# Optimization experiments

Hardware: AMD Instinct MI355X
Metric: run time of the kernel (lower is better)

Reference implementation:

```python
import jax, jax.numpy as jnp
import numpy as np


def setup_inputs() -> dict:
    key = jax.random.key(0)
    k1, k2 = jax.random.split(key)
    flow = jax.random.normal(k1, (4, 2, 256, 256), dtype=jnp.float32)   # [B,2,H,W] per-pixel flow over dt
    spike = jax.random.uniform(k2, (4, 64, 256, 256), dtype=jnp.float32)  # [B,C,H,W] spike voxel grid
    return {"flow": flow, "spike": spike}


def _splat(vals, xn, yn, H, W):
    """Forward bilinear splat of vals [H,W] to continuous coords (xn,yn) [H,W]."""
    x0 = jnp.floor(xn)
    y0 = jnp.floor(yn)
    wx = xn - x0  # fractional weights (differentiable w.r.t. flow)
    wy = yn - y0
    x0i = x0.astype(jnp.int32)
    y0i = y0.astype(jnp.int32)
    out = jnp.zeros(H * W, dtype=vals.dtype)
    corners = (
        (0, 0, (1.0 - wx) * (1.0 - wy)),
        (1, 0, wx * (1.0 - wy)),
        (0, 1, (1.0 - wx) * wy),
        (1, 1, wx * wy),
    )
    for dx, dy, w in corners:
        xi = x0i + dx
        yi = y0i + dy
        valid = (xi >= 0) & (xi < W) & (yi >= 0) & (yi < H)
        idx = jnp.clip(yi, 0, H - 1) * W + jnp.clip(xi, 0, W - 1)
        out = out.at[idx.ravel()].add(jnp.where(valid, w * vals, 0.0).ravel())
    return out.reshape(H, W)


def spike_warp_mid(spike, flow, dt):
    """Warp each time bin c by flow * (c - mid)/dt toward the middle timestamp (bilinear splat)."""
    B, C, H, W = spike.shape
    mid = (C - 1) / 2.0
    yy, xx = jnp.meshgrid(jnp.arange(H, dtype=spike.dtype),
                          jnp.arange(W, dtype=spike.dtype), indexing='ij')
    s = (jnp.arange(C, dtype=spike.dtype) - mid) / jnp.asarray(dt, spike.dtype)  # [C]
    u = flow[:, 0][:, None]  # [B,1,H,W]
    v = flow[:, 1][:, None]
    xn = xx + u * s[None, :, None, None]  # [B,C,H,W]
    yn = yy + v * s[None, :, None, None]
    splat_bc = jax.vmap(jax.vmap(lambda va, xa, ya: _splat(va, xa, ya, H, W)))
    return splat_bc(spike, xn, yn)  # [B,C,H,W]


def reference(flow, spike):
    B, C, H, W = spike.shape
    spike_warped = spike_warp_mid(spike, flow, dt=64)
    # Faithful to original: sum over BATCH dim inside per-batch loop (same each iter),
    # so loss = (B * -var) / B = -var(spike_image) with unbiased variance.
    spike_image = jnp.sum(spike_warped, axis=0)  # [C,H,W]
    loss = -jnp.var(spike_image - jnp.mean(spike_image), ddof=1)
    return loss
```

## Files before the change

kernel.cpp:

```cpp
#include <hip/hip_runtime.h>

typedef float f2 __attribute__((ext_vector_type(2)));
typedef float f4v __attribute__((ext_vector_type(4)));

constexpr int B = 4, C = 64, H = 256, W = 256;
constexpr int HW = H * W;
constexpr long long N_TOT = (long long)C * HW;

constexpr int TS = 16;
constexpr int PPS = 19;
constexpr int PPA = PPS * 18;
constexpr int OVW = 17;
constexpr int OVA = OVW * OVW;
constexpr int NBLK = 2048;

__global__ __launch_bounds__(256) void fused_kernel(
    const float* __restrict__ flow,
    const float* __restrict__ spike,
    double* __restrict__ partials) {
  __shared__ __align__(16) f4v pl01[PPA];
  __shared__ __align__(16) f4v pl23[PPA];
  __shared__ f2 uvp[PPA];
  __shared__ __align__(16) float ovf[8 * OVA];
  __shared__ double red[8];

  const int bid = blockIdx.x;
  const int part = bid >> 3;
  const int j = 7 - ((bid ^ (bid >> 3)) & 7);
  const int tx0 = (part & 15) * TS;
  const int ty0 = (part >> 4) * TS;
  const int tid = threadIdx.x;
  const int qx = tid & 15, qy = tid >> 4;
  const int wave = tid >> 6;

  {
    f4v z = {0.f, 0.f, 0.f, 0.f};
    f4v* ov4 = (f4v*)ovf;
    for (int i = tid; i < (8 * OVA) / 4; i += 256) ov4[i] = z;
  }

  f2 smv[4];
#pragma unroll
  for (int t = 0; t < 4; ++t) {
    float s = ((float)(4 * j + t) + 0.5f) * (1.0f / 64.0f);
    smv[t] = f2{-s, s};
  }
  const int cn0 = 31 - 4 * j;
  const int cp0 = 32 + 4 * j;
  const int Rj = (j >> 1) + 1;
  const int SWj = TS + 2 * Rj;
  const int SAj = SWj * SWj;
  const int sbg = (ty0 - Rj) * W + (tx0 - Rj);

  int c_rc[3];
  int c_meta[3];
#pragma unroll
  for (int k = 0; k < 3; ++k) {
    int pos = tid + 256 * k;
    bool act = pos < SAj;
    int row = act ? pos / SWj : 0;
    int col = pos - row * SWj;
    int relx = col - Rj, rely = row - Rj;
    int gy = ty0 + rely, gx = tx0 + relx;
    bool val = act & ((unsigned)gy < (unsigned)H) & ((unsigned)gx < (unsigned)W);
    bool inn = act & (relx >= -1) & (relx <= 16) & (rely >= -1) & (rely <= 16);
    c_rc[k] = (row << 8) | col;
    c_meta[k] = (int)act | ((int)val << 1) | ((int)inn << 2);
  }

  __syncthreads();

  const int qb = (qy + 1) * PPS + (qx + 1);
  f2 acc2[4];
#pragma unroll
  for (int t = 0; t < 4; ++t) acc2[t] = f2{0.f, 0.f};

  for (int bb = 0; bb < B; ++bb) {
    const float* fu = flow + (size_t)bb * 2 * HW;
    const float* fv = fu + HW;
    const float* spb = spike + (size_t)bb * C * HW;

#pragma unroll
    for (int k = 0; k < 3; ++k) {
      const int meta = c_meta[k];
      if (!(meta & 1)) continue;
      const int row = c_rc[k] >> 8, col = c_rc[k] & 255;
      const int gp = sbg + c_rc[k];
      const bool valb = (meta & 2) != 0;
      const bool innb = (meta & 4) != 0;
      float u = 0.f, v = 0.f;
      if (valb) { u = fu[gp]; v = fv[gp]; }
      const float es = fmaxf(fabsf(u), fabsf(v));
      const bool ev0 = es * smv[0].y >= 1.0f;
      const bool ev1 = es * smv[1].y >= 1.0f;
      const bool ev2 = es * smv[2].y >= 1.0f;
      const bool ev3 = es * smv[3].y >= 1.0f;
      float n0 = 0.f, n1 = 0.f, n2 = 0.f, n3 = 0.f;
      float p0 = 0.f, p1 = 0.f, p2 = 0.f, p3 = 0.f;
      if (valb && (innb || ev3)) {
        n0 = spb[(size_t)cn0 * HW + gp];
        n1 = spb[(size_t)(cn0 - 1) * HW + gp];
        n2 = spb[(size_t)(cn0 - 2) * HW + gp];
        n3 = spb[(size_t)(cn0 - 3) * HW + gp];
        p0 = spb[(size_t)cp0 * HW + gp];
        p1 = spb[(size_t)(cp0 + 1) * HW + gp];
        p2 = spb[(size_t)(cp0 + 2) * HW + gp];
        p3 = spb[(size_t)(cp0 + 3) * HW + gp];
      }
      if (innb) {
        const int relx = col - Rj, rely = row - Rj;
        const int ips = (rely + 1) * PPS + (relx + 1);
        uvp[ips] = f2{u, v};
        pl01[ips] = f4v{ev0 ? 0.f : n0, ev0 ? 0.f : p0,
                        ev1 ? 0.f : n1, ev1 ? 0.f : p1};
        pl23[ips] = f4v{ev2 ? 0.f : n2, ev2 ? 0.f : p2,
                        ev3 ? 0.f : n3, ev3 ? 0.f : p3};
      }
      if (__any(ev3)) {
        const float px = (float)(col - Rj), py = (float)(row - Rj);
        const f2 u2 = f2{u, u}, v2 = f2{v, v};
        const f2 px2 = f2{px, px}, py2 = f2{py, py};
        const float nv[4] = {n0, n1, n2, n3};
        const float pv[4] = {p0, p1, p2, p3};
#pragma unroll
        for (int tt = 0; tt < 4; ++tt) {
          const bool ev = es * smv[tt].y >= 1.0f;
          if (ev) {
            f2 xn = __builtin_elementwise_fma(u2, smv[tt], px2);
            f2 yn = __builtin_elementwise_fma(v2, smv[tt], py2);
#pragma unroll
            for (int h = 0; h < 2; ++h) {
              float x = xn[h], y = yn[h];
              float val = h ? pv[tt] : nv[tt];
              float fx = floorf(x), fy = floorf(y);
              float f = x - fx, g = y - fy;
              int X0 = (int)fx, Y0 = (int)fy;
              int ix0 = ((unsigned)X0 < 16u) ? X0 : 16;
              int ix1 = ((unsigned)(X0 + 1) < 16u) ? X0 + 1 : 16;
              int iy0 = ((unsigned)Y0 < 16u) ? Y0 : 16;
              int iy1 = ((unsigned)(Y0 + 1) < 16u) ? Y0 + 1 : 16;
              float* pl = &ovf[(2 * tt + h) * OVA];
              float w1 = f * val, w0 = val - w1;
              float g1 = g, g0 = 1.0f - g;
              atomicAdd(pl + iy0 * OVW + ix0, w0 * g0);
              atomicAdd(pl + iy0 * OVW + ix1, w1 * g0);
              atomicAdd(pl + iy1 * OVW + ix0, w0 * g1);
              atomicAdd(pl + iy1 * OVW + ix1, w1 * g1);
            }
          }
        }
      }
    }
    __syncthreads();

#pragma unroll
    for (int dy = -1; dy <= 1; ++dy) {
#pragma unroll
      for (int dx = -1; dx <= 1; ++dx) {
        const int ip = qb + dy * PPS + dx;
        const f2 uvv = uvp[ip];
        const f4v A = pl01[ip];
        const f4v Bv = pl23[ip];
        const f2 u2 = f2{uvv.x, uvv.x};
        const f2 v2 = f2{uvv.y, uvv.y};
        const f2 vals[4] = {f2{A[0], A[1]}, f2{A[2], A[3]},
                            f2{Bv[0], Bv[1]}, f2{Bv[2], Bv[3]}};
#pragma unroll
        for (int tt = 0; tt < 4; ++tt) {
          const f2 dxv = u2 * smv[tt];
          const f2 dyv = v2 * smv[tt];
          f2 wx, wy;
          if (dx < 0)      wx = __builtin_elementwise_max(dxv, f2{0.f, 0.f});
          else if (dx > 0) wx = __builtin_elementwise_max(f2{0.f, 0.f} - dxv, f2{0.f, 0.f});
          else { wx.x = 1.0f - fabsf(dxv.x); wx.y = 1.0f - fabsf(dxv.y); }
          if (dy < 0)      wy = __builtin_elementwise_max(dyv, f2{0.f, 0.f});
          else if (dy > 0) wy = __builtin_elementwise_max(f2{0.f, 0.f} - dyv, f2{0.f, 0.f});
          else { wy.x = 1.0f - fabsf(dyv.x); wy.y = 1.0f - fabsf(dyv.y); }
          acc2[tt] = __builtin_elementwise_fma(wx * wy, vals[tt], acc2[tt]);
        }
      }
    }
    if (bb + 1 < B) __syncthreads();
  }

  const int oip = qy * OVW + qx;
#pragma unroll
  for (int tt = 0; tt < 4; ++tt) {
    acc2[tt] += f2{ovf[(2 * tt) * OVA + oip], ovf[(2 * tt + 1) * OVA + oip]};
  }

  double ls = 0.0, lq = 0.0;
#pragma unroll
  for (int tt = 0; tt < 4; ++tt) {
    double a = (double)acc2[tt].x, b2 = (double)acc2[tt].y;
    ls += a + b2;
    lq += a * a + b2 * b2;
  }
  for (int off = 32; off > 0; off >>= 1) {
    ls += __shfl_down(ls, off, 64);
    lq += __shfl_down(lq, off, 64);
  }
  if ((tid & 63) == 0) { red[wave * 2] = ls; red[wave * 2 + 1] = lq; }
  __syncthreads();
  if (tid == 0) {
    partials[2 * bid] = red[0] + red[2] + red[4] + red[6];
    partials[2 * bid + 1] = red[1] + red[3] + red[5] + red[7];
  }
}

__global__ __launch_bounds__(256) void finalize_kernel(
    const double* __restrict__ partials, float* __restrict__ out) {
  double s = 0.0, q = 0.0;
  for (int i = threadIdx.x; i < NBLK; i += 256) {
    s += partials[2 * i];
    q += partials[2 * i + 1];
  }
  for (int off = 32; off > 0; off >>= 1) {
    s += __shfl_down(s, off, 64);
    q += __shfl_down(q, off, 64);
  }
  __shared__ double ss[4], qq[4];
  int lane = threadIdx.x & 63;
  int wave = threadIdx.x >> 6;
  if (lane == 0) { ss[wave] = s; qq[wave] = q; }
  __syncthreads();
  if (threadIdx.x == 0) {
    double sum = ss[0] + ss[1] + ss[2] + ss[3];
    double sq = qq[0] + qq[1] + qq[2] + qq[3];
    double n = (double)N_TOT;
    double var = (sq - sum * sum / n) / (n - 1.0);
    out[0] = (float)(-var);
  }
}

extern "C" void kernel_launch(void* const* d_in, const int* in_sizes, int n_in,
                              void* d_out, int out_size, void* d_ws, size_t ws_size,
                              hipStream_t stream) {
  const float* flow = (const float*)d_in[0];
  const float* spike = (const float*)d_in[1];
  float* out = (float*)d_out;
  double* partials = (double*)d_ws;

  fused_kernel<<<dim3(NBLK), dim3(256), 0, stream>>>(flow, spike, partials);
  finalize_kernel<<<1, dim3(256), 0, stream>>>(partials, out);
}
```

Before: 169.9 us.

## Interleave channels across blocks and prefetch next batch's flow and spike into registers

Each block now handles channels m, m+8, m+16 and m+24 on both sides of the midpoint, instead of a contiguous group of four. This gives every block the same halo (radius 4, a 24x24 staging area), so the per-block work is balanced. Spike loads are gated per channel by nested halo regions. The next batch's flow and spike values are loaded into registers right after the barrier, so the global loads overlap with the gather and accumulate phase. The cost is more register pressure, plus extra loads for the outermost channel group across the full 24x24 halo.

```diff
diff --git a/kernel.cpp b/kernel.cpp
--- a/kernel.cpp
+++ b/kernel.cpp
@@ -8,6 +8,8 @@
 constexpr long long N_TOT = (long long)C * HW;
 
 constexpr int TS = 16;
+constexpr int SW = 24;
+constexpr int SA = SW * SW;
 constexpr int PPS = 19;
 constexpr int PPA = PPS * 18;
 constexpr int OVW = 17;
@@ -25,10 +27,10 @@
   __shared__ double red[8];
 
   const int bid = blockIdx.x;
-  const int part = bid >> 3;
-  const int j = 7 - ((bid ^ (bid >> 3)) & 7);
-  const int tx0 = (part & 15) * TS;
-  const int ty0 = (part >> 4) * TS;
+  const int tile = bid >> 3;
+  const int m = bid & 7;
+  const int tx0 = (tile & 15) * TS;
+  const int ty0 = (tile >> 4) * TS;
   const int tid = threadIdx.x;
   const int qx = tid & 15, qy = tid >> 4;
   const int wave = tid >> 6;
@@ -42,90 +44,100 @@
   f2 smv[4];
 #pragma unroll
   for (int t = 0; t < 4; ++t) {
-    float s = ((float)(4 * j + t) + 0.5f) * (1.0f / 64.0f);
+    float s = ((float)(m + 8 * t) + 0.5f) * (1.0f / 64.0f);
     smv[t] = f2{-s, s};
   }
-  const int cn0 = 31 - 4 * j;
-  const int cp0 = 32 + 4 * j;
-  const int Rj = (j >> 1) + 1;
-  const int SWj = TS + 2 * Rj;
-  const int SAj = SWj * SWj;
-  const int sbg = (ty0 - Rj) * W + (tx0 - Rj);
-
-  int c_rc[3];
-  int c_meta[3];
+  const int cno[4] = {31 - m, 23 - m, 15 - m, 7 - m};
+  const int cpo[4] = {32 + m, 40 + m, 48 + m, 56 + m};
+
+  const int sbg = (ty0 - 4) * W + (tx0 - 4);
+
+  int c_rc[3], c_meta[3];
 #pragma unroll
   for (int k = 0; k < 3; ++k) {
     int pos = tid + 256 * k;
-    bool act = pos < SAj;
-    int row = act ? pos / SWj : 0;
-    int col = pos - row * SWj;
-    int relx = col - Rj, rely = row - Rj;
+    bool act = pos < SA;
+    int row = pos / SW;
+    int col = pos - row * SW;
+    int relx = col - 4, rely = row - 4;
     int gy = ty0 + rely, gx = tx0 + relx;
-    bool val = act & ((unsigned)gy < (unsigned)H) & ((unsigned)gx < (unsigned)W);
-    bool inn = act & (relx >= -1) & (relx <= 16) & (rely >= -1) & (rely <= 16);
+    bool val = act & ((unsigned)gy < 256u) & ((unsigned)gx < 256u);
+    bool i0 = ((unsigned)(relx + 1) < 18u) & ((unsigned)(rely + 1) < 18u);
+    bool i1 = ((unsigned)(relx + 2) < 20u) & ((unsigned)(rely + 2) < 20u);
+    bool i2 = ((unsigned)(relx + 3) < 22u) & ((unsigned)(rely + 3) < 22u);
     c_rc[k] = (row << 8) | col;
-    c_meta[k] = (int)act | ((int)val << 1) | ((int)inn << 2);
-  }
-
-  __syncthreads();
-
-  const int qb = (qy + 1) * PPS + (qx + 1);
-  f2 acc2[4];
-#pragma unroll
-  for (int t = 0; t < 4; ++t) acc2[t] = f2{0.f, 0.f};
-
-  for (int bb = 0; bb < B; ++bb) {
+    c_meta[k] = (int)act | ((int)val << 1) | ((int)i0 << 2) |
+                ((int)i1 << 3) | ((int)i2 << 4);
+  }
+
+  float p_u[3], p_v[3];
+  float4 p_a[3], p_b[3];
+
+  auto prefetch = [&](int bb) {
     const float* fu = flow + (size_t)bb * 2 * HW;
     const float* fv = fu + HW;
     const float* spb = spike + (size_t)bb * C * HW;
-
+#pragma unroll
+    for (int k = 0; k < 3; ++k) {
+      const int meta = c_meta[k];
+      float u = 0.f, v = 0.f;
+      float4 a = {0.f, 0.f, 0.f, 0.f};
+      float4 d = {0.f, 0.f, 0.f, 0.f};
+      if (meta & 2) {
+        const int gp = sbg + c_rc[k];
+        u = fu[gp];
+        v = fv[gp];
+        d.z = spb[(size_t)cno[3] * HW + gp];
+        d.w = spb[(size_t)cpo[3] * HW + gp];
+        if (meta & 4)  { a.x = spb[(size_t)cno[0] * HW + gp];
+                         a.y = spb[(size_t)cpo[0] * HW + gp]; }
+        if (meta & 8)  { a.z = spb[(size_t)cno[1] * HW + gp];
+                         a.w = spb[(size_t)cpo[1] * HW + gp]; }
+        if (meta & 16) { d.x = spb[(size_t)cno[2] * HW + gp];
+                         d.y = spb[(size_t)cpo[2] * HW + gp]; }
+      }
+      p_u[k] = u; p_v[k] = v; p_a[k] = a; p_b[k] = d;
+    }
+  };
+
+  prefetch(0);
+  __syncthreads();
+
+  const int qb = (qy + 1) * PPS + (qx + 1);
+  f2 acc2[4];
+#pragma unroll
+  for (int t = 0; t < 4; ++t) acc2[t] = f2{0.f, 0.f};
+
+  for (int bb = 0; bb < B; ++bb) {
 #pragma unroll
     for (int k = 0; k < 3; ++k) {
       const int meta = c_meta[k];
       if (!(meta & 1)) continue;
-      const int row = c_rc[k] >> 8, col = c_rc[k] & 255;
-      const int gp = sbg + c_rc[k];
-      const bool valb = (meta & 2) != 0;
-      const bool innb = (meta & 4) != 0;
-      float u = 0.f, v = 0.f;
-      if (valb) { u = fu[gp]; v = fv[gp]; }
+      const float u = p_u[k], v = p_v[k];
+      const float4 a = p_a[k], d = p_b[k];
       const float es = fmaxf(fabsf(u), fabsf(v));
       const bool ev0 = es * smv[0].y >= 1.0f;
       const bool ev1 = es * smv[1].y >= 1.0f;
       const bool ev2 = es * smv[2].y >= 1.0f;
       const bool ev3 = es * smv[3].y >= 1.0f;
-      float n0 = 0.f, n1 = 0.f, n2 = 0.f, n3 = 0.f;
-      float p0 = 0.f, p1 = 0.f, p2 = 0.f, p3 = 0.f;
-      if (valb && (innb || ev3)) {
-        n0 = spb[(size_t)cn0 * HW + gp];
-        n1 = spb[(size_t)(cn0 - 1) * HW + gp];
-        n2 = spb[(size_t)(cn0 - 2) * HW + gp];
-        n3 = spb[(size_t)(cn0 - 3) * HW + gp];
-        p0 = spb[(size_t)cp0 * HW + gp];
-        p1 = spb[(size_t)(cp0 + 1) * HW + gp];
-        p2 = spb[(size_t)(cp0 + 2) * HW + gp];
-        p3 = spb[(size_t)(cp0 + 3) * HW + gp];
-      }
-      if (innb) {
-        const int relx = col - Rj, rely = row - Rj;
-        const int ips = (rely + 1) * PPS + (relx + 1);
+      const int row = c_rc[k] >> 8, col = c_rc[k] & 255;
+      if (meta & 4) {
+        const int ips = (row - 3) * PPS + (col - 3);
         uvp[ips] = f2{u, v};
-        pl01[ips] = f4v{ev0 ? 0.f : n0, ev0 ? 0.f : p0,
-                        ev1 ? 0.f : n1, ev1 ? 0.f : p1};
-        pl23[ips] = f4v{ev2 ? 0.f : n2, ev2 ? 0.f : p2,
-                        ev3 ? 0.f : n3, ev3 ? 0.f : p3};
+        pl01[ips] = f4v{ev0 ? 0.f : a.x, ev0 ? 0.f : a.y,
+                        ev1 ? 0.f : a.z, ev1 ? 0.f : a.w};
+        pl23[ips] = f4v{ev2 ? 0.f : d.x, ev2 ? 0.f : d.y,
+                        ev3 ? 0.f : d.z, ev3 ? 0.f : d.w};
       }
       if (__any(ev3)) {
-        const float px = (float)(col - Rj), py = (float)(row - Rj);
+        const float px = (float)(col - 4), py = (float)(row - 4);
         const f2 u2 = f2{u, u}, v2 = f2{v, v};
         const f2 px2 = f2{px, px}, py2 = f2{py, py};
-        const float nv[4] = {n0, n1, n2, n3};
-        const float pv[4] = {p0, p1, p2, p3};
+        const float nv[4] = {a.x, a.z, d.x, d.z};
+        const float pv[4] = {a.y, a.w, d.y, d.w};
 #pragma unroll
         for (int tt = 0; tt < 4; ++tt) {
-          const bool ev = es * smv[tt].y >= 1.0f;
-          if (ev) {
+          if (es * smv[tt].y >= 1.0f) {
             f2 xn = __builtin_elementwise_fma(u2, smv[tt], px2);
             f2 yn = __builtin_elementwise_fma(v2, smv[tt], py2);
 #pragma unroll
@@ -152,6 +164,7 @@
       }
     }
     __syncthreads();
+    if (bb + 1 < B) prefetch(bb + 1);
 
 #pragma unroll
     for (int dy = -1; dy <= 1; ++dy) {
```

Measured after the change: 147.4 us. 13.2% less time.
